# Kernel tuning notes

Measured on AMD Instinct MI355X. Metric: run time of the kernel, lower is better.

The kernel has to match this reference:

```python
import jax, jax.numpy as jnp
import numpy as np

B, NC, A, C, G = 8, 6, 25200, 10, 20  # batch, cameras, anchors, classes, GT per camera
MAX_GT = 32                            # padded GT slots per camera (>= max num_gt)
LAMBDA_COORD, LAMBDA_NOOBJ, LAMBDA_OBJ, LAMBDA_CLS = 5.0, 0.5, 1.0, 1.0
IOU_THR = 0.5


def setup_inputs() -> dict:
    key = jax.random.key(0)
    k1, k2, k3, k4, k5, k6, k7 = jax.random.split(key, 7)
    cams = B * NC
    gt_cxcy = jax.random.uniform(k1, (cams * G, 2), minval=0.1, maxval=0.9)
    gt_wh = jax.random.uniform(k2, (cams * G, 2), minval=0.05, maxval=0.3)
    gt_boxes = jnp.concatenate([gt_cxcy, gt_wh], axis=-1)           # (960, 4) cxcywh, normalized
    gt_labels = jax.random.randint(k3, (cams * G,), 0, C)            # (960,)
    # per-sample cumulative end indices: [20, 40, ..., 120] per row
    start_end_idx = jnp.tile((jnp.arange(NC) + 1) * G, (B, 1)).astype(jnp.int32)
    pred_boxes = jax.random.uniform(k4, (cams, A, 4))
    # overlay noisy copies of the GT boxes on the first G anchors so positives exist
    noise = 0.01 * jax.random.normal(k5, (cams, G, 4))
    pred_boxes = pred_boxes.at[:, :G, :].set(gt_boxes.reshape(cams, G, 4) + noise)
    pred_labels = jax.random.normal(k6, (cams, A, C))
    pred_objectness = jax.random.normal(k7, (cams, A, 1))
    return {
        'pred_boxes': pred_boxes,
        'pred_labels': pred_labels,
        'pred_objectness': pred_objectness,
        'gt_boxes': gt_boxes,
        'gt_labels': gt_labels,
        'start_end_idx': start_end_idx,
    }


def _iou_cxcywh(pb, gb):
    # pb: (cams, A, 4), gb: (cams, MG, 4) -> (cams, A, MG)
    p = pb[:, :, None, :]
    g = gb[:, None, :, :]
    p1, p2 = p[..., :2] - p[..., 2:] * 0.5, p[..., :2] + p[..., 2:] * 0.5
    g1, g2 = g[..., :2] - g[..., 2:] * 0.5, g[..., :2] + g[..., 2:] * 0.5
    wh = jnp.clip(jnp.minimum(p2, g2) - jnp.maximum(p1, g1), 0.0)
    inter = wh[..., 0] * wh[..., 1]
    area_p = p[..., 2] * p[..., 3]
    area_g = g[..., 2] * g[..., 3]
    return inter / (area_p + area_g - inter + 1e-6)


def _safe_mean(x, mask):
    # per-camera mean over masked anchors; 0 if mask empty. x, mask: (cams, A)
    cnt = mask.sum(-1)
    s = (x * mask).sum(-1)
    return jnp.where(cnt > 0, s / jnp.maximum(cnt, 1.0), 0.0)


def reference(pred_boxes, pred_labels, pred_objectness, gt_boxes, gt_labels, start_end_idx):
    cams = pred_boxes.shape[0]
    s = start_end_idx.astype(jnp.int32)                              # (B, NC) per-sample cumulative
    offsets = jnp.concatenate([jnp.zeros((1,), jnp.int32), jnp.cumsum(s[:, -1])])[:-1]  # (B,)
    starts = (offsets[:, None] + jnp.concatenate(
        [jnp.zeros((s.shape[0], 1), jnp.int32), s[:, :-1]], axis=1)).reshape(-1)        # (cams,)
    ends = (offsets[:, None] + s).reshape(-1)                        # (cams,)
    ngt = ends - starts                                              # (cams,)

    k = jnp.arange(MAX_GT, dtype=jnp.int32)
    gidx = starts[:, None] + k[None, :]                              # (cams, MG)
    valid = k[None, :] < ngt[:, None]                                # (cams, MG)
    gidx_c = jnp.clip(gidx, 0, gt_boxes.shape[0] - 1)
    gtb = gt_boxes[gidx_c]                                           # (cams, MG, 4)
    gtl = gt_labels[gidx_c]                                          # (cams, MG)

    iou = _iou_cxcywh(pred_boxes, gtb)                               # (cams, A, MG)
    iou = jnp.where(valid[:, None, :], iou, -1.0)
    best_iou = iou.max(-1)                                           # (cams, A)
    best_gt = iou.argmax(-1)                                         # (cams, A)

    has_gt = ngt > 0
    pos = ((best_iou > IOU_THR) & has_gt[:, None]).astype(pred_boxes.dtype)  # (cams, A)
    neg = 1.0 - pos
    num_pos = pos.sum()
    num_neg = neg.sum()

    cam_ix = jnp.arange(cams)[:, None]
    matched_box = gtb[cam_ix, best_gt]                               # (cams, A, 4)
    matched_lbl = gtl[cam_ix, best_gt]                               # (cams, A)

    # box loss: per-camera sum of squared errors over positives, lambda_coord weighted
    box_se = ((pred_boxes - matched_box) ** 2).sum(-1)               # (cams, A)
    box_loss_c = LAMBDA_COORD * (box_se * pos).sum(-1)               # (cams,)

    # objectness BCE-with-logits: target 1 -> softplus(-x); target 0 -> softplus(x)
    o = pred_objectness[..., 0]                                      # (cams, A)
    obj_loss_c = LAMBDA_OBJ * _safe_mean(jax.nn.softplus(-o), pos)
    noobj_loss_c = LAMBDA_NOOBJ * _safe_mean(jax.nn.softplus(o), neg)

    # classification CE over positives (per-camera mean)
    logp = jax.nn.log_softmax(pred_labels, axis=-1)                  # (cams, A, C)
    ce = -jnp.take_along_axis(logp, matched_lbl[..., None], axis=-1)[..., 0]
    cls_loss_c = LAMBDA_CLS * _safe_mean(ce, pos)

    box_loss = jnp.where(num_pos > 0, box_loss_c.sum() / jnp.maximum(num_pos, 1.0), 0.0)
    obj_loss = jnp.where(num_pos > 0, obj_loss_c.sum() / jnp.maximum(num_pos, 1.0), 0.0)
    cls_loss = jnp.where(num_pos > 0, cls_loss_c.sum() / jnp.maximum(num_pos, 1.0), 0.0)
    noobj_loss = jnp.where(num_neg > 0, noobj_loss_c.sum() / jnp.maximum(num_neg, 1.0), 0.0)
    total_loss = box_loss + obj_loss + noobj_loss + cls_loss
    return jnp.stack([total_loss, box_loss, obj_loss, noobj_loss, cls_loss])
```

## Files before the change

### kernel.cpp

```cpp
#include <hip/hip_runtime.h>
#include <math.h>

#define NCAMS 48
#define NC_   6
#define A_    25200
#define C_    10
#define MAXGT 32
#define L_COORD 5.0f
#define L_NOOBJ 0.5f

#define BLOCK  256
#define APT    4
#define CHUNK  (BLOCK * APT)
#define NCHUNK ((A_ + CHUNK - 1) / CHUNK)

__device__ __forceinline__ float softplus_f(float x) {
    return fmaxf(x, 0.0f) + log1pf(expf(-fabsf(x)));
}

__global__ __launch_bounds__(BLOCK)
void yolo_phase1(const float* __restrict__ pred_boxes,
                 const float* __restrict__ pred_labels,
                 const float* __restrict__ pred_obj,
                 const float* __restrict__ gt_boxes,
                 const int*   __restrict__ gt_labels,
                 const int*   __restrict__ se,
                 int total_gt,
                 float* __restrict__ partials)
{
    const int cam   = blockIdx.y;
    const int chunk = blockIdx.x;
    const int tid   = threadIdx.x;

    __shared__ float4 s_corner[MAXGT];
    __shared__ float4 s_orig[MAXGT];
    __shared__ float  s_area[MAXGT];
    __shared__ int    s_lbl[MAXGT];
    __shared__ float  s_red[BLOCK / 64][6];

    const int b  = cam / NC_;
    const int nc = cam - b * NC_;
    int off = 0;
    for (int bb = 0; bb < b; ++bb) off += se[bb * NC_ + (NC_ - 1)];
    const int start = off + (nc ? se[b * NC_ + nc - 1] : 0);
    const int end   = off + se[b * NC_ + nc];
    int ngt = end - start;
    if (ngt < 0) ngt = 0;
    if (ngt > MAXGT) ngt = MAXGT;

    if (tid < ngt) {
        int gi = start + tid;
        gi = min(max(gi, 0), total_gt - 1);
        float4 gb = ((const float4*)gt_boxes)[gi];
        float hw = gb.z * 0.5f, hh = gb.w * 0.5f;
        s_corner[tid] = make_float4(gb.x - hw, gb.y - hh, gb.x + hw, gb.y + hh);
        s_orig[tid]   = gb;
        s_area[tid]   = gb.z * gb.w;
        s_lbl[tid]    = gt_labels[gi];
    }
    __syncthreads();

    const int base = chunk * CHUNK;
    const float4* pb4 = (const float4*)pred_boxes;

    int   aidx[APT];
    bool  valid[APT];
    float p1x[APT], p1y[APT], p2x[APT], p2y[APT], pa[APT];
    float bn[APT], bd[APT];
    int   bk[APT];
    float o[APT];
    float4 p[APT];

    #pragma unroll
    for (int j = 0; j < APT; ++j) {
        const int a = base + j * BLOCK + tid;
        valid[j] = (a < A_);
        const int ac = valid[j] ? a : (A_ - 1);
        const int idx = cam * A_ + ac;
        aidx[j] = idx;
        p[j] = pb4[idx];
        o[j] = pred_obj[idx];
        const float hw = p[j].z * 0.5f, hh = p[j].w * 0.5f;
        p1x[j] = p[j].x - hw; p1y[j] = p[j].y - hh;
        p2x[j] = p[j].x + hw; p2y[j] = p[j].y + hh;
        pa[j]  = p[j].z * p[j].w + 1e-6f;
        bn[j] = -1.0f; bd[j] = 1.0f; bk[j] = 0;
    }

    auto iou_step = [&](int k) {
        const float4 g = s_corner[k];
        const float ga = s_area[k];
        #pragma unroll
        for (int j = 0; j < APT; ++j) {
            const float wx = fmaxf(fminf(p2x[j], g.z) - fmaxf(p1x[j], g.x), 0.0f);
            const float wy = fmaxf(fminf(p2y[j], g.w) - fmaxf(p1y[j], g.y), 0.0f);
            const float inter = wx * wy;
            const float d = pa[j] + (ga - inter);
            const bool better = inter * bd[j] > bn[j] * d;
            bn[j] = better ? inter : bn[j];
            bd[j] = better ? d     : bd[j];
            bk[j] = better ? k     : bk[j];
        }
    };

    if (ngt == 20) {
        #pragma unroll
        for (int k = 0; k < 20; ++k) iou_step(k);
    } else {
        for (int k = 0; k < ngt; ++k) iou_step(k);
    }

    float pos_cnt = 0.f, neg_cnt = 0.f;
    float box_acc = 0.f, spp_acc = 0.f, spn_acc = 0.f, ce_acc = 0.f;

    #pragma unroll
    for (int j = 0; j < APT; ++j) {
        if (!valid[j]) continue;
        if (bn[j] > 0.5f * bd[j]) {
            pos_cnt += 1.0f;
            const float4 mb = s_orig[bk[j]];
            const float dx = p[j].x - mb.x, dy = p[j].y - mb.y;
            const float dz = p[j].z - mb.z, dw = p[j].w - mb.w;
            box_acc += dx * dx + dy * dy + dz * dz + dw * dw;
            spp_acc += softplus_f(-o[j]);
            const float* lg = pred_labels + aidx[j] * C_;
            float m = lg[0];
            #pragma unroll
            for (int i = 1; i < C_; ++i) m = fmaxf(m, lg[i]);
            float sexp = 0.f;
            #pragma unroll
            for (int i = 0; i < C_; ++i) sexp += expf(lg[i] - m);
            ce_acc += -(lg[s_lbl[bk[j]]] - m - logf(sexp));
        } else {
            neg_cnt += 1.0f;
            spn_acc += softplus_f(o[j]);
        }
    }

    float v[6] = {pos_cnt, neg_cnt, box_acc, spp_acc, spn_acc, ce_acc};
    #pragma unroll
    for (int i = 0; i < 6; ++i) {
        float x = v[i];
        for (int s = 32; s; s >>= 1) x += __shfl_down(x, s, 64);
        v[i] = x;
    }
    if ((tid & 63) == 0) {
        const int w = tid >> 6;
        #pragma unroll
        for (int i = 0; i < 6; ++i) s_red[w][i] = v[i];
    }
    __syncthreads();
    if (tid == 0) {
        float* outp = partials + (size_t)(cam * NCHUNK + chunk) * 8;
        #pragma unroll
        for (int i = 0; i < 6; ++i)
            outp[i] = s_red[0][i] + s_red[1][i] + s_red[2][i] + s_red[3][i];
    }
}

__global__ void yolo_phase2(const float* __restrict__ partials,
                            float* __restrict__ out)
{
    const int t = threadIdx.x;
    float box_sum = 0.f, obj_sum = 0.f, noobj_sum = 0.f, cls_sum = 0.f;
    float np_ = 0.f, nn_ = 0.f;

    if (t < NCAMS) {
        float pp = 0.f, n = 0.f, bx = 0.f, sp = 0.f, sn = 0.f, ce = 0.f;
        for (int h = 0; h < NCHUNK; ++h) {
            const float* q = partials + (size_t)(t * NCHUNK + h) * 8;
            pp += q[0]; n  += q[1]; bx += q[2];
            sp += q[3]; sn += q[4]; ce += q[5];
        }
        box_sum   = L_COORD * bx;
        obj_sum   = (pp > 0.f) ? sp / fmaxf(pp, 1.0f) : 0.f;
        cls_sum   = (pp > 0.f) ? ce / fmaxf(pp, 1.0f) : 0.f;
        noobj_sum = L_NOOBJ * ((n > 0.f) ? sn / fmaxf(n, 1.0f) : 0.f);
        np_ = pp; nn_ = n;
    }
    for (int s = 32; s; s >>= 1) {
        box_sum   += __shfl_down(box_sum, s, 64);
        obj_sum   += __shfl_down(obj_sum, s, 64);
        noobj_sum += __shfl_down(noobj_sum, s, 64);
        cls_sum   += __shfl_down(cls_sum, s, 64);
        np_       += __shfl_down(np_, s, 64);
        nn_       += __shfl_down(nn_, s, 64);
    }
    if (t == 0) {
        const float box_loss   = (np_ > 0.f) ? box_sum / fmaxf(np_, 1.0f) : 0.f;
        const float obj_loss   = (np_ > 0.f) ? obj_sum / fmaxf(np_, 1.0f) : 0.f;
        const float cls_loss   = (np_ > 0.f) ? cls_sum / fmaxf(np_, 1.0f) : 0.f;
        const float noobj_loss = (nn_ > 0.f) ? noobj_sum / fmaxf(nn_, 1.0f) : 0.f;
        const float total = box_loss + obj_loss + noobj_loss + cls_loss;
        out[0] = total;
        out[1] = box_loss;
        out[2] = obj_loss;
        out[3] = noobj_loss;
        out[4] = cls_loss;
    }
}

extern "C" void kernel_launch(void* const* d_in, const int* in_sizes, int n_in,
                              void* d_out, int out_size, void* d_ws, size_t ws_size,
                              hipStream_t stream) {
    const float* pred_boxes  = (const float*)d_in[0];
    const float* pred_labels = (const float*)d_in[1];
    const float* pred_obj    = (const float*)d_in[2];
    const float* gt_boxes    = (const float*)d_in[3];
    const int*   gt_labels   = (const int*)d_in[4];
    const int*   se          = (const int*)d_in[5];
    const int total_gt = in_sizes[3] / 4;

    float* partials = (float*)d_ws;

    dim3 grid(NCHUNK, NCAMS);
    yolo_phase1<<<grid, BLOCK, 0, stream>>>(pred_boxes, pred_labels, pred_obj,
                                            gt_boxes, gt_labels, se,
                                            total_gt, partials);
    yolo_phase2<<<1, 64, 0, stream>>>(partials, (float*)d_out);
}
```

Before: 124.7 us.

## Replace per-GT argmax IoU tracking with threshold max test plus rare rescan

Turns the test IoU>0.5 into 3*inter - (area_g+eps) > area_p, so the main loop over GT boxes keeps one running max per anchor and no longer tracks best numerator, denominator and index. Only anchors that pass the test redo the full IoU argmax over the GT boxes to find the matched box, and they reload the pred box from global memory. This cuts ALU work and register pressure in the hot loop, in exchange for a divergent rescan on the few positive anchors. Edge cases near the threshold may round slightly differently from the reference.

Measured after the change: 127.8 us. 2.4% more time.

```diff
diff --git a/kernel.cpp b/kernel.cpp
--- a/kernel.cpp
+++ b/kernel.cpp
@@ -32,9 +32,9 @@
     const int chunk = blockIdx.x;
     const int tid   = threadIdx.x;
 
-    __shared__ float4 s_corner[MAXGT];
-    __shared__ float4 s_orig[MAXGT];
-    __shared__ float  s_area[MAXGT];
+    __shared__ float4 s_g[MAXGT];
+    __shared__ float  s_thr[MAXGT];
+    __shared__ float4 s_gb[MAXGT];
     __shared__ int    s_lbl[MAXGT];
     __shared__ float  s_red[BLOCK / 64][6];
 
@@ -45,69 +45,56 @@
     const int start = off + (nc ? se[b * NC_ + nc - 1] : 0);
     const int end   = off + se[b * NC_ + nc];
     int ngt = end - start;
-    if (ngt < 0) ngt = 0;
-    if (ngt > MAXGT) ngt = MAXGT;
+    ngt = min(max(ngt, 0), MAXGT);
 
     if (tid < ngt) {
-        int gi = start + tid;
-        gi = min(max(gi, 0), total_gt - 1);
-        float4 gb = ((const float4*)gt_boxes)[gi];
-        float hw = gb.z * 0.5f, hh = gb.w * 0.5f;
-        s_corner[tid] = make_float4(gb.x - hw, gb.y - hh, gb.x + hw, gb.y + hh);
-        s_orig[tid]   = gb;
-        s_area[tid]   = gb.z * gb.w;
-        s_lbl[tid]    = gt_labels[gi];
+        const int gi = min(max(start + tid, 0), total_gt - 1);
+        const float4 gb = ((const float4*)gt_boxes)[gi];
+        const float hw = gb.z * 0.5f, hh = gb.w * 0.5f;
+        s_g[tid]   = make_float4(gb.x - hw, gb.y - hh, gb.x + hw, gb.y + hh);
+        s_thr[tid] = gb.z * gb.w + 1e-6f;
+        s_gb[tid]  = gb;
+        s_lbl[tid] = gt_labels[gi];
     }
     __syncthreads();
 
     const int base = chunk * CHUNK;
     const float4* pb4 = (const float4*)pred_boxes;
 
+    bool  valid[APT];
     int   aidx[APT];
-    bool  valid[APT];
-    float p1x[APT], p1y[APT], p2x[APT], p2y[APT], pa[APT];
-    float bn[APT], bd[APT];
-    int   bk[APT];
-    float o[APT];
-    float4 p[APT];
+    float p1x[APT], p1y[APT], p2x[APT], p2y[APT], pa[APT], o[APT], m[APT];
 
     #pragma unroll
     for (int j = 0; j < APT; ++j) {
         const int a = base + j * BLOCK + tid;
         valid[j] = (a < A_);
-        const int ac = valid[j] ? a : (A_ - 1);
-        const int idx = cam * A_ + ac;
+        const int idx = cam * A_ + (valid[j] ? a : (A_ - 1));
         aidx[j] = idx;
-        p[j] = pb4[idx];
+        const float4 p = pb4[idx];
         o[j] = pred_obj[idx];
-        const float hw = p[j].z * 0.5f, hh = p[j].w * 0.5f;
-        p1x[j] = p[j].x - hw; p1y[j] = p[j].y - hh;
-        p2x[j] = p[j].x + hw; p2y[j] = p[j].y + hh;
-        pa[j]  = p[j].z * p[j].w + 1e-6f;
-        bn[j] = -1.0f; bd[j] = 1.0f; bk[j] = 0;
-    }
-
-    auto iou_step = [&](int k) {
-        const float4 g = s_corner[k];
-        const float ga = s_area[k];
+        const float hw = p.z * 0.5f, hh = p.w * 0.5f;
+        p1x[j] = p.x - hw; p1y[j] = p.y - hh;
+        p2x[j] = p.x + hw; p2y[j] = p.y + hh;
+        pa[j]  = p.z * p.w;
+        m[j]   = -1e30f;
+    }
+
+    auto step = [&](int k) {
+        const float4 g  = s_g[k];
+        const float thr = s_thr[k];
         #pragma unroll
         for (int j = 0; j < APT; ++j) {
             const float wx = fmaxf(fminf(p2x[j], g.z) - fmaxf(p1x[j], g.x), 0.0f);
             const float wy = fmaxf(fminf(p2y[j], g.w) - fmaxf(p1y[j], g.y), 0.0f);
-            const float inter = wx * wy;
-            const float d = pa[j] + (ga - inter);
-            const bool better = inter * bd[j] > bn[j] * d;
-            bn[j] = better ? inter : bn[j];
-            bd[j] = better ? d     : bd[j];
-            bk[j] = better ? k     : bk[j];
+            m[j] = fmaxf(m[j], fmaf(3.0f, wx * wy, -thr));
         }
     };
-
     if (ngt == 20) {
-        #pragma unroll
-        for (int k = 0; k < 20; ++k) iou_step(k);
+        #pragma unroll 5
+        for (int k = 0; k < 20; ++k) step(k);
     } else {
-        for (int k = 0; k < ngt; ++k) iou_step(k);
+        for (int k = 0; k < ngt; ++k) step(k);
     }
 
     float pos_cnt = 0.f, neg_cnt = 0.f;
@@ -116,21 +103,31 @@
     #pragma unroll
     for (int j = 0; j < APT; ++j) {
         if (!valid[j]) continue;
-        if (bn[j] > 0.5f * bd[j]) {
+        if (m[j] > pa[j]) {
             pos_cnt += 1.0f;
-            const float4 mb = s_orig[bk[j]];
-            const float dx = p[j].x - mb.x, dy = p[j].y - mb.y;
-            const float dz = p[j].z - mb.z, dw = p[j].w - mb.w;
+            float best = -1.0f; int bk = 0;
+            for (int k = 0; k < ngt; ++k) {
+                const float4 g = s_g[k];
+                const float wx = fmaxf(fminf(p2x[j], g.z) - fmaxf(p1x[j], g.x), 0.0f);
+                const float wy = fmaxf(fminf(p2y[j], g.w) - fmaxf(p1y[j], g.y), 0.0f);
+                const float inter = wx * wy;
+                const float iou = inter / (pa[j] + (s_thr[k] - inter));
+                if (iou > best) { best = iou; bk = k; }
+            }
+            const float4 p  = pb4[aidx[j]];
+            const float4 gb = s_gb[bk];
+            const float dx = p.x - gb.x, dy = p.y - gb.y;
+            const float dz = p.z - gb.z, dw = p.w - gb.w;
             box_acc += dx * dx + dy * dy + dz * dz + dw * dw;
             spp_acc += softplus_f(-o[j]);
-            const float* lg = pred_labels + aidx[j] * C_;
-            float m = lg[0];
+            const float* lg = pred_labels + (size_t)aidx[j] * C_;
+            float mx = lg[0];
             #pragma unroll
-            for (int i = 1; i < C_; ++i) m = fmaxf(m, lg[i]);
+            for (int i = 1; i < C_; ++i) mx = fmaxf(mx, lg[i]);
             float sexp = 0.f;
             #pragma unroll
-            for (int i = 0; i < C_; ++i) sexp += expf(lg[i] - m);
-            ce_acc += -(lg[s_lbl[bk[j]]] - m - logf(sexp));
+            for (int i = 0; i < C_; ++i) sexp += expf(lg[i] - mx);
+            ce_acc += -(lg[s_lbl[bk]] - mx - logf(sexp));
         } else {
             neg_cnt += 1.0f;
             spn_acc += softplus_f(o[j]);
```
